# Kernel optimization log

Measured on AMD Instinct MI355X. Metric: run time of the kernel, lower is better.

The kernel has to match this reference:

```python
import jax, jax.numpy as jnp
import numpy as np

B, N, DX, DR, H, DOUT = 4, 384, 2, 128, 128, 64


def setup_inputs() -> dict:
    key = jax.random.key(0)
    ks = jax.random.split(key, 6)
    return {
        "r": jax.random.normal(ks[0], (B, DR), dtype=jnp.float32),
        "x_ctx": jax.random.normal(ks[1], (B, N, DX), dtype=jnp.float32),
        "y_ctx": jax.random.normal(ks[2], (B, N, 1), dtype=jnp.float32),
        "x_trg": jax.random.normal(ks[3], (B, 256, DX), dtype=jnp.float32),
        "W1": jax.random.normal(ks[4], (DX + DR, H), dtype=jnp.float32) * (1.0 / np.sqrt(DX + DR)),
        "b1": jnp.zeros((H,), dtype=jnp.float32),
        "W2": jax.random.normal(ks[5], (H, DOUT), dtype=jnp.float32) * (1.0 / np.sqrt(H)),
        "b2": jnp.zeros((DOUT,), dtype=jnp.float32),
    }


def reference(r, x_ctx, y_ctx, x_trg, W1, b1, W2, b2):
    # Pairwise differences over the context set: [B, N, N, DX]
    x_diff = x_ctx[:, :, None, :] - x_ctx[:, None, :, :]
    # Broadcast the context representation over the pair grid: [B, N, N, DR]
    n = x_ctx.shape[1]
    r_rep = jnp.broadcast_to(r[:, None, None, :], (r.shape[0], n, n, r.shape[-1]))
    # Concat then pointwise deepset MLP (Linear -> ReLU -> Linear)
    z = jnp.concatenate([x_diff, r_rep], axis=-1)  # [B, N, N, DX+DR]
    h = jax.nn.relu(jnp.einsum('bnmd,dh->bnmh', z, W1) + b1)
    out = jnp.einsum('bnmh,ho->bnmo', h, W2) + b2  # [B, N, N, DOUT]
    return out
```

## Files before the change

### kernel.cpp

```cpp
#include <hip/hip_runtime.h>


typedef __attribute__((ext_vector_type(8))) __bf16 bf16x8;
typedef __attribute__((ext_vector_type(4))) float f32x4;
typedef __attribute__((ext_vector_type(2))) float f32x2;

#define B_    4
#define N_    384
#define H_    128
#define DOUT_ 64

__global__ __launch_bounds__(128, 3) void te_fused(
    const float* __restrict__ r, const float* __restrict__ xctx,
    const float* __restrict__ W1, const float* __restrict__ b1,
    const float* __restrict__ W2, const float* __restrict__ b2,
    float* __restrict__ out)
{
    __shared__ __align__(16) float xs[N_ * 2];
    __shared__ __align__(16) float cs[H_];
    __shared__ __align__(16) float tbuf[2][2][16][64];

    const int tid  = threadIdx.x;
    const int w    = tid >> 6, lane = tid & 63;
    const int g    = lane >> 4, rl = lane & 15;

    const int bid = blockIdx.x;
    const int b = bid / N_, n = bid - b * N_;

    {
        float acc = b1[tid];
        const float* wc = W1 + 2 * H_ + tid;
        const float* rb = r + b * 128;
        #pragma unroll 8
        for (int d = 0; d < 128; ++d) acc = fmaf(rb[d], wc[d * H_], acc);
        cs[tid] = acc;
    }
    {
        const float* xb = xctx + b * (N_ * 2);
        *reinterpret_cast<f32x4*>(&xs[tid * 4]) =
            *reinterpret_cast<const f32x4*>(xb + tid * 4);
        if (tid < 64)
            *reinterpret_cast<f32x4*>(&xs[(128 + tid) * 4]) =
                *reinterpret_cast<const f32x4*>(xb + (128 + tid) * 4);
    }

    bf16x8 w2f[2][4];
    #pragma unroll
    for (int ot = 0; ot < 2; ++ot) {
        const float* wp = W2 + w * 32 + ot * 16 + rl;
        #pragma unroll
        for (int ks = 0; ks < 4; ++ks)
            #pragma unroll
            for (int jj = 0; jj < 8; ++jj) {
                const int kk = ks * 32 + ((jj >> 2) << 4) + (g << 2) + (jj & 3);
                w2f[ot][ks][jj] = (__bf16)wp[kk * DOUT_];
            }
    }

    f32x4 w1a[4][2], w1b[4][2], cf[4][2], b2f[2];
    #pragma unroll
    for (int ks = 0; ks < 4; ++ks)
        #pragma unroll
        for (int hh = 0; hh < 2; ++hh) {
            const int kk = ks * 32 + hh * 16 + (g << 2);
            w1a[ks][hh] = *reinterpret_cast<const f32x4*>(W1 + kk);
            w1b[ks][hh] = *reinterpret_cast<const f32x4*>(W1 + H_ + kk);
        }
    #pragma unroll
    for (int ot = 0; ot < 2; ++ot)
        b2f[ot] = *reinterpret_cast<const f32x4*>(b2 + w * 32 + ot * 16 + (g << 2));

    __syncthreads();

    #pragma unroll
    for (int ks = 0; ks < 4; ++ks)
        #pragma unroll
        for (int hh = 0; hh < 2; ++hh)
            cf[ks][hh] = *reinterpret_cast<const f32x4*>(&cs[ks * 32 + hh * 16 + (g << 2)]);

    const float x0n = xs[2 * n], x1n = xs[2 * n + 1];
    float* const outn = out + ((size_t)(b * N_ + n)) * N_ * DOUT_;
    const int ob2 = tid & 15;
    const int mr0 = tid >> 4;

    for (int tp = 0; tp < 12; ++tp) {
        const int s = tp & 1;

        #pragma unroll
        for (int half = 0; half < 2; ++half) {
            const int m = tp * 32 + half * 16 + rl;
            const f32x2 xp = *reinterpret_cast<const f32x2*>(&xs[2 * m]);
            const float dx0 = x0n - xp[0], dx1 = x1n - xp[1];

            bf16x8 hf[4];
            #pragma unroll
            for (int ks = 0; ks < 4; ++ks)
                #pragma unroll
                for (int hh = 0; hh < 2; ++hh)
                    #pragma unroll
                    for (int j = 0; j < 4; ++j) {
                        float hp = fmaf(dx1, w1b[ks][hh][j],
                                   fmaf(dx0, w1a[ks][hh][j], cf[ks][hh][j]));
                        hf[ks][hh * 4 + j] = (__bf16)(hp > 0.f ? hp : 0.f);
                    }

            f32x4 acc0 = b2f[0], acc1 = b2f[1];
            #pragma unroll
            for (int ks = 0; ks < 4; ++ks) {
                acc0 = __builtin_amdgcn_mfma_f32_16x16x32_bf16(w2f[0][ks], hf[ks], acc0, 0, 0, 0);
                acc1 = __builtin_amdgcn_mfma_f32_16x16x32_bf16(w2f[1][ks], hf[ks], acc1, 0, 0, 0);
            }

            {
                const int ob0 = (w << 3) | g;
                *reinterpret_cast<f32x4*>(&tbuf[s][half][rl][(ob0 ^ rl) << 2]) = acc0;
                const int ob1 = (w << 3) | 4 | g;
                *reinterpret_cast<f32x4*>(&tbuf[s][half][rl][(ob1 ^ rl) << 2]) = acc1;
            }
        }

        __syncthreads();

        float* const onp = outn + (size_t)(tp * 32) * DOUT_;
        #pragma unroll
        for (int p = 0; p < 4; ++p) {
            const int sub = p >> 1;
            const int mr  = mr0 + ((p & 1) << 3);
            f32x4 rv = *reinterpret_cast<const f32x4*>(&tbuf[s][sub][mr][(ob2 ^ mr) << 2]);
            *reinterpret_cast<f32x4*>(onp + (size_t)(sub * 16 + mr) * DOUT_ + (ob2 << 2)) = rv;
        }
    }
}

extern "C" void kernel_launch(void* const* d_in, const int* in_sizes, int n_in,
                              void* d_out, int out_size, void* d_ws, size_t ws_size,
                              hipStream_t stream)
{
    const float* r    = (const float*)d_in[0];
    const float* xctx = (const float*)d_in[1];
    const float* W1 = (const float*)d_in[4];
    const float* b1 = (const float*)d_in[5];
    const float* W2 = (const float*)d_in[6];
    const float* b2 = (const float*)d_in[7];
    float* out = (float*)d_out;

    hipLaunchKernelGGL(te_fused, dim3(B_ * N_), dim3(128), 0, stream,
                       r, xctx, W1, b1, W2, b2, out);
}
```

Before: 40.71 us.

## Store MFMA outputs directly to global and use fp16 dot2 for first layer

Removes the shared-memory transpose buffer and the per-iteration barrier: each lane now writes its MFMA accumulator fragments straight to global memory as 16-byte stores. The first-layer pointwise math is switched from two fp32 FMAs to one packed fp16 dot2 instruction per hidden unit, with W1 rows and the x differences converted to half. This cuts LDS traffic, barriers and ALU work. In exchange the global stores are less contiguous per wavefront, and the half-precision inputs lose some accuracy.

```diff
diff --git a/kernel.cpp b/kernel.cpp
--- a/kernel.cpp
+++ b/kernel.cpp
@@ -4,6 +4,15 @@
 typedef __attribute__((ext_vector_type(8))) __bf16 bf16x8;
 typedef __attribute__((ext_vector_type(4))) float f32x4;
 typedef __attribute__((ext_vector_type(2))) float f32x2;
+typedef _Float16 half_t;
+typedef __attribute__((ext_vector_type(2))) half_t half2_t;
+
+#if __has_builtin(__builtin_amdgcn_fdot2)
+#define FDOT2(a, b, c) __builtin_amdgcn_fdot2((a), (b), (c), false)
+#else
+#define FDOT2(a, b, c) fmaf((float)(a)[0], (float)(b)[0], \
+                       fmaf((float)(a)[1], (float)(b)[1], (c)))
+#endif
 
 #define B_    4
 #define N_    384
@@ -18,7 +27,6 @@
 {
     __shared__ __align__(16) float xs[N_ * 2];
     __shared__ __align__(16) float cs[H_];
-    __shared__ __align__(16) float tbuf[2][2][16][64];
 
     const int tid  = threadIdx.x;
     const int w    = tid >> 6, lane = tid & 63;
@@ -40,8 +48,8 @@
         *reinterpret_cast<f32x4*>(&xs[tid * 4]) =
             *reinterpret_cast<const f32x4*>(xb + tid * 4);
         if (tid < 64)
-            *reinterpret_cast<f32x4*>(&xs[(128 + tid) * 4]) =
-                *reinterpret_cast<const f32x4*>(xb + (128 + tid) * 4);
+            *reinterpret_cast<f32x4*>(&xs[512 + tid * 4]) =
+                *reinterpret_cast<const f32x4*>(xb + 512 + tid * 4);
     }
 
     bf16x8 w2f[2][4];
@@ -57,21 +65,27 @@
             }
     }
 
-    f32x4 w1a[4][2], w1b[4][2], cf[4][2], b2f[2];
+    half2_t w1p[4][2][4];
     #pragma unroll
     for (int ks = 0; ks < 4; ++ks)
         #pragma unroll
         for (int hh = 0; hh < 2; ++hh) {
-            const int kk = ks * 32 + hh * 16 + (g << 2);
-            w1a[ks][hh] = *reinterpret_cast<const f32x4*>(W1 + kk);
-            w1b[ks][hh] = *reinterpret_cast<const f32x4*>(W1 + H_ + kk);
+            const int kk0 = ks * 32 + hh * 16 + (g << 2);
+            const f32x4 a0 = *reinterpret_cast<const f32x4*>(W1 + kk0);
+            const f32x4 a1 = *reinterpret_cast<const f32x4*>(W1 + H_ + kk0);
+            #pragma unroll
+            for (int j = 0; j < 4; ++j)
+                w1p[ks][hh][j] = half2_t{(half_t)a0[j], (half_t)a1[j]};
         }
+
+    f32x4 b2f[2];
     #pragma unroll
     for (int ot = 0; ot < 2; ++ot)
         b2f[ot] = *reinterpret_cast<const f32x4*>(b2 + w * 32 + ot * 16 + (g << 2));
 
     __syncthreads();
 
+    f32x4 cf[4][2];
     #pragma unroll
     for (int ks = 0; ks < 4; ++ks)
         #pragma unroll
@@ -79,56 +93,41 @@
             cf[ks][hh] = *reinterpret_cast<const f32x4*>(&cs[ks * 32 + hh * 16 + (g << 2)]);
 
     const float x0n = xs[2 * n], x1n = xs[2 * n + 1];
-    float* const outn = out + ((size_t)(b * N_ + n)) * N_ * DOUT_;
-    const int ob2 = tid & 15;
-    const int mr0 = tid >> 4;
+    float* const outn = out + ((size_t)(b * N_ + n)) * (N_ * DOUT_) + w * 32;
 
-    for (int tp = 0; tp < 12; ++tp) {
-        const int s = tp & 1;
+    auto tile = [&](int mt, f32x4& A0, f32x4& A1) {
+        const int m = mt * 16 + rl;
+        const f32x2 xp = *reinterpret_cast<const f32x2*>(&xs[2 * m]);
+        const half2_t dxp = {(half_t)(x0n - xp[0]), (half_t)(x1n - xp[1])};
 
+        bf16x8 hf[4];
         #pragma unroll
-        for (int half = 0; half < 2; ++half) {
-            const int m = tp * 32 + half * 16 + rl;
-            const f32x2 xp = *reinterpret_cast<const f32x2*>(&xs[2 * m]);
-            const float dx0 = x0n - xp[0], dx1 = x1n - xp[1];
+        for (int ks = 0; ks < 4; ++ks)
+            #pragma unroll
+            for (int hh = 0; hh < 2; ++hh)
+                #pragma unroll
+                for (int j = 0; j < 4; ++j) {
+                    float hp = FDOT2(dxp, w1p[ks][hh][j], cf[ks][hh][j]);
+                    hf[ks][hh * 4 + j] = (__bf16)(hp > 0.f ? hp : 0.f);
+                }
 
-            bf16x8 hf[4];
-            #pragma unroll
-            for (int ks = 0; ks < 4; ++ks)
-                #pragma unroll
-                for (int hh = 0; hh < 2; ++hh)
-                    #pragma unroll
-                    for (int j = 0; j < 4; ++j) {
-                        float hp = fmaf(dx1, w1b[ks][hh][j],
-                                   fmaf(dx0, w1a[ks][hh][j], cf[ks][hh][j]));
-                        hf[ks][hh * 4 + j] = (__bf16)(hp > 0.f ? hp : 0.f);
-                    }
-
-            f32x4 acc0 = b2f[0], acc1 = b2f[1];
-            #pragma unroll
-            for (int ks = 0; ks < 4; ++ks) {
-                acc0 = __builtin_amdgcn_mfma_f32_16x16x32_bf16(w2f[0][ks], hf[ks], acc0, 0, 0, 0);
-                acc1 = __builtin_amdgcn_mfma_f32_16x16x32_bf16(w2f[1][ks], hf[ks], acc1, 0, 0, 0);
-            }
-
-            {
-                const int ob0 = (w << 3) | g;
-                *reinterpret_cast<f32x4*>(&tbuf[s][half][rl][(ob0 ^ rl) << 2]) = acc0;
-                const int ob1 = (w << 3) | 4 | g;
-                *reinterpret_cast<f32x4*>(&tbuf[s][half][rl][(ob1 ^ rl) << 2]) = acc1;
-            }
+        A0 = __builtin_amdgcn_mfma_f32_16x16x32_bf16(w2f[0][0], hf[0], b2f[0], 0, 0, 0);
+        A1 = __builtin_amdgcn_mfma_f32_16x16x32_bf16(w2f[1][0], hf[0], b2f[1], 0, 0, 0);
+        #pragma unroll
+        for (int ks = 1; ks < 4; ++ks) {
+            A0 = __builtin_amdgcn_mfma_f32_16x16x32_bf16(w2f[0][ks], hf[ks], A0, 0, 0, 0);
+            A1 = __builtin_amdgcn_mfma_f32_16x16x32_bf16(w2f[1][ks], hf[ks], A1, 0, 0, 0);
         }
 
-        __syncthreads();
+        float* onp = outn + mt * (16 * DOUT_) + rl * DOUT_ + (g << 2);
+        *reinterpret_cast<f32x4*>(onp)      = A0;
+        *reinterpret_cast<f32x4*>(onp + 16) = A1;
+    };
 
-        float* const onp = outn + (size_t)(tp * 32) * DOUT_;
-        #pragma unroll
-        for (int p = 0; p < 4; ++p) {
-            const int sub = p >> 1;
-            const int mr  = mr0 + ((p & 1) << 3);
-            f32x4 rv = *reinterpret_cast<const f32x4*>(&tbuf[s][sub][mr][(ob2 ^ mr) << 2]);
-            *reinterpret_cast<f32x4*>(onp + (size_t)(sub * 16 + mr) * DOUT_ + (ob2 << 2)) = rv;
-        }
+    f32x4 aA0, aA1, aB0, aB1;
+    for (int mt2 = 0; mt2 < 12; ++mt2) {
+        tile(2 * mt2,     aA0, aA1);
+        tile(2 * mt2 + 1, aB0, aB1);
     }
 }
 
```

Result: slower. 49.41 us (+21.4%).
